# Kernel optimization log

Measured on AMD Instinct MI355X. Metric: run time of the kernel, lower is better.

Reference implementation:

```python
import jax, jax.numpy as jnp
import numpy as np


def setup_inputs() -> dict:
    key = jax.random.key(0)
    k1, k2 = jax.random.split(key)
    N = 8192
    preds = jax.random.normal(k1, (N,), dtype=jnp.float32)
    targets = jax.random.normal(k2, (N,), dtype=jnp.float32)
    return {"preds": preds, "targets": targets}


def reference(preds, targets):
    n = preds.shape[0]
    # torch.std is unbiased (ddof=1)
    margin = 0.25 * jnp.std(targets, ddof=1)
    # broadcasted all-pairs differences: [N, N]
    tdiff = targets[:, None] - targets[None, :]
    pdiff = preds[:, None] - preds[None, :]
    loss = jnp.maximum(-jnp.sign(tdiff) * pdiff + margin, 0.0)
    # only pairs with i < j (strict upper triangle)
    mask = jnp.triu(jnp.ones((n, n), dtype=bool), k=1)
    num_pairs = n * (n - 1) // 2
    total = jnp.sum(jnp.where(mask, loss, 0.0))
    return total / num_pairs
```

## Files before the change

kernel.cpp:

```cpp
#include <hip/hip_runtime.h>

#define NT    512
#define SPLIT 2
#define ROWS  8
#define NW    (NT / 64)

__device__ __forceinline__ float pair_loss(float tt, float pp, float tj, float pj, float margin) {
    float td = tt - tj;
    float pd = pp - pj;
    float cs = copysignf(1.0f, td);
    return fmaxf(fmaf(-cs, pd, margin), 0.0f);
}

__device__ __forceinline__ void do_j(float tj, float pj, const float* tg, const float* pg,
                                     float margin, float* av) {
    #pragma unroll
    for (int k = 0; k < ROWS; ++k) av[k] += pair_loss(tg[k], pg[k], tj, pj, margin);
}

__global__ __launch_bounds__(NT, 8)
void pair_kernel(const float* __restrict__ preds, const float* __restrict__ targets,
                 double* __restrict__ partials, int N)
{
    const int tid = threadIdx.x, lane = tid & 63, wave = tid >> 6;
    __shared__ float  sred[2 * NW];
    __shared__ double redd[NW];

    float margin;
    {
        float s = 0.0f, s2 = 0.0f;
        const int n4 = N >> 2;
        const float4* t4 = (const float4*)targets;
        for (int i = tid; i < n4; i += NT) {
            float4 v = t4[i];
            s  += v.x + v.y + v.z + v.w;
            s2 += v.x * v.x + v.y * v.y + v.z * v.z + v.w * v.w;
        }
        for (int i = (n4 << 2) + tid; i < N; i += NT) { float t = targets[i]; s += t; s2 += t * t; }
        #pragma unroll
        for (int off = 32; off; off >>= 1) { s += __shfl_xor(s, off, 64); s2 += __shfl_xor(s2, off, 64); }
        if (lane == 0) { sred[wave] = s; sred[NW + wave] = s2; }
        __syncthreads();
        float S = 0.0f, S2 = 0.0f;
        #pragma unroll
        for (int w = 0; w < NW; ++w) { S += sred[w]; S2 += sred[NW + w]; }
        float mean = S / (float)N;
        float var  = (S2 - (float)N * mean * mean) / (float)(N - 1);
        margin = 0.25f * sqrtf(fmaxf(var, 0.0f));
    }

    const int G = N >> 3;
    const int P = G >> 1;
    const int NB = (int)gridDim.x;
    const int sub = (int)(blockIdx.x & (SPLIT - 1));
    const int pairblk = (int)(blockIdx.x >> 1);
    const int PSTRIDE = NB >> 1;

    float av[ROWS];
    #pragma unroll
    for (int k = 0; k < ROWS; ++k) av[k] = 0.0f;
    float extra = 0.0f;

    for (int p = pairblk; p < P; p += PSTRIDE) {
        #pragma unroll
        for (int side = 0; side < 2; ++side) {
            const int gg = side ? (G - 1 - p) : p;
            const int i0 = gg << 3;
            float tg[ROWS], pg[ROWS];
            #pragma unroll
            for (int k = 0; k < ROWS; ++k) { tg[k] = targets[i0 + k]; pg[k] = preds[i0 + k]; }

            if (sub == side && tid < 64) {
                int ii = tid >> 3, jj = tid & 7;
                if (ii < jj) {
                    float td = tg[ii] - tg[jj], pd = pg[ii] - pg[jj];
                    float cs = (td > 0.0f) ? 1.0f : ((td < 0.0f) ? -1.0f : 0.0f);
                    extra += fmaxf(fmaf(-cs, pd, margin), 0.0f);
                }
            }

            const int lo = i0 + ROWS;
            const int len = N - lo;
            const int len4 = len >> 2;
            const float4* tj4 = (const float4*)(targets + lo);
            const float4* pj4 = (const float4*)(preds + lo);
            for (int idx = sub * NT + tid; idx < len4; idx += NT * SPLIT) {
                float4 tv = tj4[idx];
                float4 pv = pj4[idx];
                do_j(tv.x, pv.x, tg, pg, margin, av);
                do_j(tv.y, pv.y, tg, pg, margin, av);
                do_j(tv.z, pv.z, tg, pg, margin, av);
                do_j(tv.w, pv.w, tg, pg, margin, av);
            }
            for (int j = lo + (len4 << 2) + sub * NT + tid; j < N; j += NT * SPLIT) {
                do_j(targets[j], preds[j], tg, pg, margin, av);
            }
        }
    }

    if (pairblk == 0) {
        if (G & 1) {
            const int i0 = (G >> 1) << 3;
            for (int k = 0; k < ROWS && i0 + k < N; ++k) {
                const int i = i0 + k;
                for (int j = i + 1 + sub * NT + tid; j < N; j += NT * SPLIT) {
                    float td = targets[i] - targets[j], pd = preds[i] - preds[j];
                    float cs = (td > 0.0f) ? 1.0f : ((td < 0.0f) ? -1.0f : 0.0f);
                    extra += fmaxf(fmaf(-cs, pd, margin), 0.0f);
                }
            }
        }
        for (int i = G << 3; i < N; ++i) {
            for (int j = i + 1 + sub * NT + tid; j < N; j += NT * SPLIT) {
                float td = targets[i] - targets[j], pd = preds[i] - preds[j];
                float cs = (td > 0.0f) ? 1.0f : ((td < 0.0f) ? -1.0f : 0.0f);
                extra += fmaxf(fmaf(-cs, pd, margin), 0.0f);
            }
        }
    }

    double tot = (double)extra;
    #pragma unroll
    for (int k = 0; k < ROWS; ++k) tot += (double)av[k];
    #pragma unroll
    for (int off = 32; off; off >>= 1) tot += __shfl_down(tot, off, 64);
    __syncthreads();
    if (lane == 0) redd[wave] = tot;
    __syncthreads();
    if (tid == 0) {
        double bt = 0.0;
        for (int w = 0; w < NW; ++w) bt += redd[w];
        partials[blockIdx.x] = bt;
    }
}

__global__ __launch_bounds__(256)
void finalize_kernel(const double* __restrict__ partials, int nparts,
                     float* __restrict__ out, double inv_pairs)
{
    __shared__ double red[4];
    const int tid = threadIdx.x, lane = tid & 63, wave = tid >> 6;
    double s = 0.0;
    for (int i = tid; i < nparts; i += 256) s += partials[i];
    #pragma unroll
    for (int off = 32; off; off >>= 1) s += __shfl_down(s, off, 64);
    if (lane == 0) red[wave] = s;
    __syncthreads();
    if (tid == 0) {
        double t = 0.0;
        for (int w = 0; w < 4; ++w) t += red[w];
        out[0] = (float)(t * inv_pairs);
    }
}

extern "C" void kernel_launch(void* const* d_in, const int* in_sizes, int n_in,
                              void* d_out, int out_size, void* d_ws, size_t ws_size,
                              hipStream_t stream) {
    const float* preds   = (const float*)d_in[0];
    const float* targets = (const float*)d_in[1];
    float* out = (float*)d_out;
    int N = in_sizes[0];

    double* partials = (double*)d_ws;

    const int G = N >> 3;
    const int P = G >> 1;
    int NB = (P > 0 ? P : 1) * SPLIT;
    if (NB > 1024) NB = 1024;

    const double inv_pairs = 2.0 / ((double)N * (double)(N - 1));
    pair_kernel<<<NB, NT, 0, stream>>>(preds, targets, partials, N);
    finalize_kernel<<<1, 256, 0, stream>>>(partials, NB, out, inv_pairs);
}
```

Baseline: 18.71 us.

## Fuse finalize into pair kernel via hierarchical atomic last-block reduction

Removes the separate finalize kernel launch. Each block publishes its partial with a release atomic and bumps a two-level counter tree, and the last block to arrive sums all partials and writes the output. Block size also drops from 512 to 256 threads with a fixed 1024-block grid. The counters are never reset; the modulo-32 checks rely on exactly 1024 blocks per launch so they keep working across repeated calls. Since NB is fixed at 1024 instead of derived from N, the grid no longer adapts to the input size.

```diff
diff --git a/kernel.cpp b/kernel.cpp
--- a/kernel.cpp
+++ b/kernel.cpp
@@ -1,6 +1,7 @@
 #include <hip/hip_runtime.h>
 
-#define NT    512
+#define NT    256
+#define NB    1024
 #define SPLIT 2
 #define ROWS  8
 #define NW    (NT / 64)
@@ -18,13 +19,18 @@
     for (int k = 0; k < ROWS; ++k) av[k] += pair_loss(tg[k], pg[k], tj, pj, margin);
 }
 
-__global__ __launch_bounds__(NT, 8)
+__global__ __launch_bounds__(NT, 4)
 void pair_kernel(const float* __restrict__ preds, const float* __restrict__ targets,
-                 double* __restrict__ partials, int N)
+                 double* __restrict__ partials,
+                 unsigned int* __restrict__ leafcnt,
+                 unsigned int* __restrict__ rootcnt,
+                 float* __restrict__ out, int N, double inv_pairs)
 {
     const int tid = threadIdx.x, lane = tid & 63, wave = tid >> 6;
+    const int bid = (int)blockIdx.x;
     __shared__ float  sred[2 * NW];
     __shared__ double redd[NW];
+    __shared__ int sflag;
 
     float margin;
     {
@@ -51,9 +57,8 @@
 
     const int G = N >> 3;
     const int P = G >> 1;
-    const int NB = (int)gridDim.x;
-    const int sub = (int)(blockIdx.x & (SPLIT - 1));
-    const int pairblk = (int)(blockIdx.x >> 1);
+    const int sub = bid & (SPLIT - 1);
+    const int pairblk = bid >> 1;
     const int PSTRIDE = NB >> 1;
 
     float av[ROWS];
@@ -127,29 +132,36 @@
     __syncthreads();
     if (lane == 0) redd[wave] = tot;
     __syncthreads();
+
     if (tid == 0) {
         double bt = 0.0;
         for (int w = 0; w < NW; ++w) bt += redd[w];
-        partials[blockIdx.x] = bt;
+        __hip_atomic_exchange(&partials[bid], bt, __ATOMIC_RELEASE, __HIP_MEMORY_SCOPE_AGENT);
+        const unsigned g = (unsigned)bid >> 5;
+        unsigned lv = __hip_atomic_fetch_add(&leafcnt[g], 1u, __ATOMIC_ACQ_REL, __HIP_MEMORY_SCOPE_AGENT);
+        int f = 0;
+        if ((lv & 31u) == 31u) {
+            unsigned rv = __hip_atomic_fetch_add(rootcnt, 1u, __ATOMIC_ACQ_REL, __HIP_MEMORY_SCOPE_AGENT);
+            if ((rv & 31u) == 31u) f = 1;
+        }
+        sflag = f;
     }
-}
+    __syncthreads();
 
-__global__ __launch_bounds__(256)
-void finalize_kernel(const double* __restrict__ partials, int nparts,
-                     float* __restrict__ out, double inv_pairs)
-{
-    __shared__ double red[4];
-    const int tid = threadIdx.x, lane = tid & 63, wave = tid >> 6;
-    double s = 0.0;
-    for (int i = tid; i < nparts; i += 256) s += partials[i];
-    #pragma unroll
-    for (int off = 32; off; off >>= 1) s += __shfl_down(s, off, 64);
-    if (lane == 0) red[wave] = s;
-    __syncthreads();
-    if (tid == 0) {
-        double t = 0.0;
-        for (int w = 0; w < 4; ++w) t += red[w];
-        out[0] = (float)(t * inv_pairs);
+    if (sflag != 0) {
+        double s = 0.0;
+        for (int i = tid; i < NB; i += NT)
+            s += __hip_atomic_fetch_add(&partials[i], 0.0, __ATOMIC_ACQUIRE, __HIP_MEMORY_SCOPE_AGENT);
+        #pragma unroll
+        for (int off = 32; off; off >>= 1) s += __shfl_down(s, off, 64);
+        __syncthreads();
+        if (lane == 0) redd[wave] = s;
+        __syncthreads();
+        if (tid == 0) {
+            double t = 0.0;
+            for (int w = 0; w < NW; ++w) t += redd[w];
+            out[0] = (float)(t * inv_pairs);
+        }
     }
 }
 
@@ -161,14 +173,11 @@
     float* out = (float*)d_out;
     int N = in_sizes[0];
 
-    double* partials = (double*)d_ws;
-
-    const int G = N >> 3;
-    const int P = G >> 1;
-    int NB = (P > 0 ? P : 1) * SPLIT;
-    if (NB > 1024) NB = 1024;
+    double*       partials = (double*)d_ws;
+    unsigned int* leafcnt  = (unsigned int*)((char*)d_ws + NB * sizeof(double));
+    unsigned int* rootcnt  = leafcnt + 32;
 
     const double inv_pairs = 2.0 / ((double)N * (double)(N - 1));
-    pair_kernel<<<NB, NT, 0, stream>>>(preds, targets, partials, N);
-    finalize_kernel<<<1, 256, 0, stream>>>(partials, NB, out, inv_pairs);
+    pair_kernel<<<NB, NT, 0, stream>>>(preds, targets, partials, leafcnt, rootcnt,
+                                       out, N, inv_pairs);
 }
```

New measurement: 37.18 us. 1.99x slower.
